# Kernel tuning notes

Hardware: AMD Instinct MI355X
Metric: run time of the kernel (lower is better)

The kernel has to match this reference:

```python
import jax, jax.numpy as jnp
import numpy as np

N = 16384        # num_nodes (64 graphs x 256 nodes, consecutive blocks)
G = 64           # num_graphs = len(nodes_per_graph)
GENES = 12132    # num_genes (hardcoded in source)
E = 262144       # edges, avg degree 16
PER = 256        # nodes per graph


def setup_inputs() -> dict:
    key = jax.random.key(0)
    ks = jax.random.split(key, 12)
    x = jax.random.normal(ks[0], (N, GENES), dtype=jnp.float32)
    edge_index = jax.random.randint(ks[1], (2, E), 0, N, dtype=jnp.int32)
    # node i belongs to graph i // PER  (consecutive-block partition as in the source loop)
    graph_ids = jnp.repeat(jnp.arange(G, dtype=jnp.int32), PER)
    node_scales = jax.random.uniform(ks[2], (GENES,), dtype=jnp.float32, minval=0.5, maxval=1.5)
    gcn_weight = jax.random.normal(ks[3], (GENES, G), dtype=jnp.float32) / np.float32(np.sqrt(GENES))
    gcn_bias = jax.random.normal(ks[4], (G,), dtype=jnp.float32) * 0.01
    w1 = jax.random.normal(ks[5], (G, N), dtype=jnp.float32) / np.float32(np.sqrt(N))   # to_graph_layer [out,in]
    b1 = jax.random.normal(ks[6], (G,), dtype=jnp.float32) * 0.01
    final_means = jax.random.normal(ks[7], (G,), dtype=jnp.float32)
    final_scales = jax.random.uniform(ks[8], (G,), dtype=jnp.float32, minval=0.5, maxval=1.5)
    w2 = jax.random.normal(ks[9], (1, G), dtype=jnp.float32) / np.float32(np.sqrt(G))   # to_final_layer
    b2 = jax.random.normal(ks[10], (1,), dtype=jnp.float32) * 0.01
    return {
        "x": x, "edge_index": edge_index, "graph_ids": graph_ids,
        "node_scales": node_scales, "gcn_weight": gcn_weight, "gcn_bias": gcn_bias,
        "w1": w1, "b1": b1, "final_means": final_means, "final_scales": final_scales,
        "w2": w2, "b2": b2,
    }


def reference(x, edge_index, graph_ids, node_scales, gcn_weight, gcn_bias,
              w1, b1, final_means, final_scales, w2, b2):
    n = x.shape[0]
    x = x / node_scales                              # [N, GENES]
    xw = x @ gcn_weight                              # [N, G]  GCNConv linear (normalize=False)
    src, dst = edge_index[0], edge_index[1]
    # message passing: sum x_j over in-edges; '+ xw' realizes the explicitly-added self loops
    agg = jax.ops.segment_sum(xw[src], dst, num_segments=n) + xw + gcn_bias  # [N, G]
    # per-graph gather: node i takes column graph_ids[i] (vectorized form of the source loop)
    selected = jnp.take_along_axis(agg, graph_ids[:, None], axis=1)[:, 0]    # [N]
    # NOTE: the (selected - graph_means)/graph_scales in the source is dead code
    # (immediately overwritten by `x = selected_outputs`), so it is omitted.
    h = w1 @ selected + b1                           # [G]
    h = (h - final_means) / final_scales
    out = w2 @ h + b2                                # [1]
    return jax.nn.sigmoid(out)
```

## Files before the change

### kernel.cpp

```cpp
#include <hip/hip_runtime.h>
#include <hip/hip_bf16.h>

typedef unsigned short u16;
typedef unsigned int   u32;
typedef __attribute__((ext_vector_type(8))) short bf16x8;
typedef __attribute__((ext_vector_type(4))) float f32x4;
typedef __attribute__((ext_vector_type(4))) u32   u32x4;

#define GENES  12132
#define KPAD   12160
#define NROW   16384
#define GCOL   64
#define BM     64
#define BK     64
#define CHUNKS 190
#define KTAIL  12096

__device__ __forceinline__ u32 pack_hi(float x, float y) {
  return __builtin_amdgcn_perm(__float_as_uint(y), __float_as_uint(x), 0x07060302u);
}
__device__ __forceinline__ u32 pack_lo(float x, float y) {
  float lx = x - __uint_as_float(__float_as_uint(x) & 0xFFFF0000u);
  float ly = y - __uint_as_float(__float_as_uint(y) & 0xFFFF0000u);
  return pack_hi(lx, ly);
}
__device__ __forceinline__ void cvt8(const float* __restrict__ p, bf16x8& h8, bf16x8& l8) {
  const f32x4 a = *(const f32x4*)p;
  const f32x4 b = *(const f32x4*)(p + 4);
  u32x4 hv = { pack_hi(a[0], a[1]), pack_hi(a[2], a[3]),
               pack_hi(b[0], b[1]), pack_hi(b[2], b[3]) };
  u32x4 lv = { pack_lo(a[0], a[1]), pack_lo(a[2], a[3]),
               pack_lo(b[0], b[1]), pack_lo(b[2], b[3]) };
  h8 = __builtin_bit_cast(bf16x8, hv);
  l8 = __builtin_bit_cast(bf16x8, lv);
}

__device__ __forceinline__ void gload16(const void* g, void* l) {
  __builtin_amdgcn_global_load_lds(
      (const __attribute__((address_space(1))) void*)g,
      (__attribute__((address_space(3))) void*)l, 16, 0, 0);
}

__global__ __launch_bounds__(256) void prep_all(
    const float* __restrict__ gw, const float* __restrict__ ns,
    const float* __restrict__ x,
    u16* __restrict__ Wth, u16* __restrict__ Wtl,
    float* __restrict__ xpad, float* __restrict__ hbuf) {
  const int bid = blockIdx.x;
  const int t   = threadIdx.x;
  if (bid < CHUNKS) {
    __shared__ u16 th[64 * 72];
    __shared__ u16 tl[64 * 72];
    const int k0 = bid * 64;
#pragma unroll
    for (int i = 0; i < 16; ++i) {
      int idx = i * 256 + t;
      int k = idx >> 6, c = idx & 63;
      int gk = k0 + k;
      float wv = 0.f;
      if (gk < GENES) wv = gw[(size_t)gk * GCOL + c] / ns[gk];
      u32 u = __float_as_uint(wv);
      float lf = wv - __uint_as_float(u & 0xFFFF0000u);
      th[c * 72 + k] = (u16)(u >> 16);
      tl[c * 72 + k] = (u16)(__float_as_uint(lf) >> 16);
    }
    __syncthreads();
    const int c  = t >> 2;
    const int kk = (t & 3) * 16;
    uint4 a0 = *(const uint4*)(th + c * 72 + kk);
    uint4 a1 = *(const uint4*)(th + c * 72 + kk + 8);
    uint4 b0 = *(const uint4*)(tl + c * 72 + kk);
    uint4 b1 = *(const uint4*)(tl + c * 72 + kk + 8);
    *(uint4*)(Wth + (size_t)c * KPAD + k0 + kk)     = a0;
    *(uint4*)(Wth + (size_t)c * KPAD + k0 + kk + 8) = a1;
    *(uint4*)(Wtl + (size_t)c * KPAD + k0 + kk)     = b0;
    *(uint4*)(Wtl + (size_t)c * KPAD + k0 + kk + 8) = b1;
  } else {
    int i = (bid - CHUNKS) * 256 + t;
    int row = i >> 6, col = i & 63;
    float v = 0.f;
    if (col < GENES - KTAIL) v = x[(size_t)row * GENES + KTAIL + col];
    xpad[i] = v;
    if (bid == CHUNKS && t < 64) hbuf[t] = 0.f;
  }
}

__global__ __launch_bounds__(512, 2) void gemm_kernel(
    const float* __restrict__ x, const float* __restrict__ xpad,
    const u16* __restrict__ Wth, const u16* __restrict__ Wtl,
    const float* __restrict__ gb,
    float* __restrict__ xw, float* __restrict__ sel) {
  __shared__ float Abuf[4][BM * BK];
  __shared__ u16   Bbuf[4][2][64 * BK];

  const int t    = threadIdx.x;
  const int W    = t >> 6;
  const int lane = t & 63;
  const int r0   = blockIdx.x * BM;

  const int arow0 = t >> 4,         acol0 = t & 15;
  const int arow1 = (512 + t) >> 4, acol1 = (512 + t) & 15;
  const int asrc0 = ((((acol0 >> 1) ^ (arow0 & 7)) << 1) | (acol0 & 1)) << 2;
  const int asrc1 = ((((acol1 >> 1) ^ (arow1 & 7)) << 1) | (acol1 & 1)) << 2;
  const int bc   = t >> 3;
  const int bsrc = ((t & 7) ^ (bc & 7)) << 3;

  const int wm = W >> 1, wn = W & 1;
  const int lr = lane & 15;
  const int kg = lane >> 4;
  const int arow = wm * 16 + lr;
  const int aridx0 = arow * 64 + (((0 * 4 + kg) ^ (arow & 7)) << 3);
  const int aridx1 = arow * 64 + (((1 * 4 + kg) ^ (arow & 7)) << 3);
  int bidx[2][2];
#pragma unroll
  for (int n2 = 0; n2 < 2; ++n2) {
    int c = (wn * 2 + n2) * 16 + lr;
#pragma unroll
    for (int s = 0; s < 2; ++s)
      bidx[n2][s] = c * 64 + (((s * 4 + kg) ^ (c & 7)) << 3);
  }

  f32x4 acc[2];
  acc[0] = (f32x4){0.f, 0.f, 0.f, 0.f};
  acc[1] = (f32x4){0.f, 0.f, 0.f, 0.f};

  auto STAGE = [&](int buf, int ch) {
    const float* Ab;
    size_t astr;
    int kof;
    if (ch < CHUNKS - 1) { Ab = x;    astr = GENES; kof = ch * BK; }
    else                 { Ab = xpad; astr = 64;    kof = 0;       }
    const int k0 = ch * BK;
    gload16(Ab + (size_t)(r0 + arow0) * astr + kof + asrc0, &Abuf[buf][(W * 64) * 4]);
    gload16(Ab + (size_t)(r0 + arow1) * astr + kof + asrc1, &Abuf[buf][(512 + W * 64) * 4]);
    gload16(Wth + (size_t)bc * KPAD + k0 + bsrc, &Bbuf[buf][0][(W * 64) * 8]);
    gload16(Wtl + (size_t)bc * KPAD + k0 + bsrc, &Bbuf[buf][1][(W * 64) * 8]);
  };

  auto COMPUTE = [&](int p) {
    bf16x8 ah0, al0, ah1, al1;
    cvt8(&Abuf[p][aridx0], ah0, al0);
    cvt8(&Abuf[p][aridx1], ah1, al1);
#pragma unroll
    for (int n2 = 0; n2 < 2; ++n2) {
      bf16x8 bh0 = *(const bf16x8*)&Bbuf[p][0][bidx[n2][0]];
      bf16x8 bl0 = *(const bf16x8*)&Bbuf[p][1][bidx[n2][0]];
      acc[n2] = __builtin_amdgcn_mfma_f32_16x16x32_bf16(ah0, bh0, acc[n2], 0, 0, 0);
      acc[n2] = __builtin_amdgcn_mfma_f32_16x16x32_bf16(al0, bh0, acc[n2], 0, 0, 0);
      acc[n2] = __builtin_amdgcn_mfma_f32_16x16x32_bf16(ah0, bl0, acc[n2], 0, 0, 0);
      bf16x8 bh1 = *(const bf16x8*)&Bbuf[p][0][bidx[n2][1]];
      bf16x8 bl1 = *(const bf16x8*)&Bbuf[p][1][bidx[n2][1]];
      acc[n2] = __builtin_amdgcn_mfma_f32_16x16x32_bf16(ah1, bh1, acc[n2], 0, 0, 0);
      acc[n2] = __builtin_amdgcn_mfma_f32_16x16x32_bf16(al1, bh1, acc[n2], 0, 0, 0);
      acc[n2] = __builtin_amdgcn_mfma_f32_16x16x32_bf16(ah1, bl1, acc[n2], 0, 0, 0);
    }
  };

  STAGE(0, 0);
  STAGE(1, 1);
  STAGE(2, 2);

  for (int ch = 0; ch < CHUNKS - 3; ++ch) {
    asm volatile("s_waitcnt vmcnt(8)" ::: "memory");
    __builtin_amdgcn_s_barrier();
    STAGE((ch + 3) & 3, ch + 3);
    COMPUTE(ch & 3);
  }
  asm volatile("s_waitcnt vmcnt(8)" ::: "memory");
  __builtin_amdgcn_s_barrier();
  COMPUTE((CHUNKS - 3) & 3);
  asm volatile("s_waitcnt vmcnt(4)" ::: "memory");
  __builtin_amdgcn_s_barrier();
  COMPUTE((CHUNKS - 2) & 3);
  asm volatile("s_waitcnt vmcnt(0)" ::: "memory");
  __builtin_amdgcn_s_barrier();
  COMPUTE((CHUNKS - 1) & 3);

  const int orow = r0 + wm * 16 + kg * 4;
#pragma unroll
  for (int n2 = 0; n2 < 2; ++n2) {
    const int col = (wn * 2 + n2) * 16 + lr;
#pragma unroll
    for (int j = 0; j < 4; ++j)
      xw[(size_t)(orow + j) * GCOL + col] = acc[n2][j];
  }
  const int g = blockIdx.x >> 2;
  if (wn == (g >> 5) && lr == (g & 15)) {
    f32x4 av = ((g >> 4) & 1) ? acc[1] : acc[0];
    float bias = gb[g];
#pragma unroll
    for (int j = 0; j < 4; ++j)
      sel[orow + j] = av[j] + bias;
  }
}

__global__ __launch_bounds__(256) void edge_kernel(
    const int* __restrict__ ei, const float* __restrict__ xw,
    float* __restrict__ sel, int E) {
  int e = blockIdx.x * 256 + threadIdx.x;
  if (e < E) {
    int s = ei[e];
    int d = ei[E + e];
    int g = d >> 8;
    atomicAdd(&sel[d], xw[(size_t)s * GCOL + g]);
  }
}

__global__ __launch_bounds__(256) void hreduce_kernel(
    const float* __restrict__ w1, const float* __restrict__ sel,
    float* __restrict__ hbuf) {
  const int k = blockIdx.x >> 2;
  const int q = blockIdx.x & 3;
  const int t = threadIdx.x;
  const float4* wr = reinterpret_cast<const float4*>(w1 + (size_t)k * NROW);
  const float4* sv = reinterpret_cast<const float4*>(sel);
  float sum = 0.f;
#pragma unroll
  for (int i = 0; i < 4; ++i) {
    int idx = q * 1024 + i * 256 + t;
    float4 a = wr[idx];
    float4 b = sv[idx];
    sum += a.x * b.x + a.y * b.y + a.z * b.z + a.w * b.w;
  }
#pragma unroll
  for (int off = 32; off > 0; off >>= 1) sum += __shfl_down(sum, off, 64);
  __shared__ float wsum[4];
  if ((t & 63) == 0) wsum[t >> 6] = sum;
  __syncthreads();
  if (t == 0) atomicAdd(&hbuf[k], wsum[0] + wsum[1] + wsum[2] + wsum[3]);
}

__global__ void finalize_kernel(
    const float* __restrict__ hbuf, const float* __restrict__ b1,
    const float* __restrict__ fm, const float* __restrict__ fs,
    const float* __restrict__ w2, const float* __restrict__ b2,
    float* __restrict__ out) {
  int t = threadIdx.x;
  float h  = hbuf[t] + b1[t];
  float hn = (h - fm[t]) / fs[t];
  float v  = w2[t] * hn;
#pragma unroll
  for (int off = 32; off > 0; off >>= 1) v += __shfl_down(v, off, 64);
  if (t == 0) {
    float z = v + b2[0];
    out[0] = 1.f / (1.f + expf(-z));
  }
}

extern "C" void kernel_launch(void* const* d_in, const int* in_sizes, int n_in,
                              void* d_out, int out_size, void* d_ws, size_t ws_size,
                              hipStream_t stream) {
  const float* x    = (const float*)d_in[0];
  const int*   ei   = (const int*)d_in[1];
  const float* ns   = (const float*)d_in[3];
  const float* gw   = (const float*)d_in[4];
  const float* gb   = (const float*)d_in[5];
  const float* w1   = (const float*)d_in[6];
  const float* b1   = (const float*)d_in[7];
  const float* fm   = (const float*)d_in[8];
  const float* fs   = (const float*)d_in[9];
  const float* w2   = (const float*)d_in[10];
  const float* b2   = (const float*)d_in[11];
  float* out = (float*)d_out;

  const int E = in_sizes[1] / 2;

  float* ws   = (float*)d_ws;
  float* xw   = ws;
  float* sel  = xw + (size_t)NROW * GCOL;
  float* hbuf = sel + NROW;
  u16*   Wth  = (u16*)(hbuf + 64);
  u16*   Wtl  = Wth + (size_t)GCOL * KPAD;
  float* xpad = (float*)(Wtl + (size_t)GCOL * KPAD);

  hipLaunchKernelGGL(prep_all, dim3(CHUNKS + NROW * 64 / 256), dim3(256), 0, stream,
                     gw, ns, x, Wth, Wtl, xpad, hbuf);
  hipLaunchKernelGGL(gemm_kernel, dim3(NROW / BM), dim3(512), 0, stream,
                     x, xpad, Wth, Wtl, gb, xw, sel);
  hipLaunchKernelGGL(edge_kernel, dim3((E + 255) / 256), dim3(256), 0, stream,
                     ei, xw, sel, E);
  hipLaunchKernelGGL(hreduce_kernel, dim3(GCOL * 4), dim3(256), 0, stream,
                     w1, sel, hbuf);
  hipLaunchKernelGGL(finalize_kernel, dim3(1), dim3(64), 0, stream,
                     hbuf, b1, fm, fs, w2, b2, out);
}
```

Baseline: 341.9 us.

## Replace LDS-pipelined GEMM with split-K single-wave direct-load kernel plus reduction

The GEMM is rewritten so each single-wave block computes a full 64x64 output tile for one fifth of the K dimension. It loads A and B straight from global memory into registers with no LDS staging or barriers. A new reduce kernel sums the five partial results, writes xw and computes the per-graph selected values with bias. The aim is more parallel blocks and no barrier overhead, at the cost of extra partial-sum traffic, one more launch, and uncoalesced per-lane global loads with no LDS reuse.

```diff
diff --git a/kernel.cpp b/kernel.cpp
--- a/kernel.cpp
+++ b/kernel.cpp
@@ -11,10 +11,10 @@
 #define KPAD   12160
 #define NROW   16384
 #define GCOL   64
-#define BM     64
-#define BK     64
-#define CHUNKS 190
 #define KTAIL  12096
+#define CHUNKS32 380
+#define KSPLIT 5
+#define CPW    76
 
 __device__ __forceinline__ u32 pack_hi(float x, float y) {
   return __builtin_amdgcn_perm(__float_as_uint(y), __float_as_uint(x), 0x07060302u);
@@ -35,12 +35,6 @@
   l8 = __builtin_bit_cast(bf16x8, lv);
 }
 
-__device__ __forceinline__ void gload16(const void* g, void* l) {
-  __builtin_amdgcn_global_load_lds(
-      (const __attribute__((address_space(1))) void*)g,
-      (__attribute__((address_space(3))) void*)l, 16, 0, 0);
-}
-
 __global__ __launch_bounds__(256) void prep_all(
     const float* __restrict__ gw, const float* __restrict__ ns,
     const float* __restrict__ x,
@@ -48,7 +42,7 @@
     float* __restrict__ xpad, float* __restrict__ hbuf) {
   const int bid = blockIdx.x;
   const int t   = threadIdx.x;
-  if (bid < CHUNKS) {
+  if (bid < KPAD / 64) {
     __shared__ u16 th[64 * 72];
     __shared__ u16 tl[64 * 72];
     const int k0 = bid * 64;
@@ -76,122 +70,96 @@
     *(uint4*)(Wtl + (size_t)c * KPAD + k0 + kk)     = b0;
     *(uint4*)(Wtl + (size_t)c * KPAD + k0 + kk + 8) = b1;
   } else {
-    int i = (bid - CHUNKS) * 256 + t;
+    int i = (bid - KPAD / 64) * 256 + t;
     int row = i >> 6, col = i & 63;
     float v = 0.f;
     if (col < GENES - KTAIL) v = x[(size_t)row * GENES + KTAIL + col];
     xpad[i] = v;
-    if (bid == CHUNKS && t < 64) hbuf[t] = 0.f;
-  }
-}
-
-__global__ __launch_bounds__(512, 2) void gemm_kernel(
+    if (bid == KPAD / 64 && t < 64) hbuf[t] = 0.f;
+  }
+}
+
+__global__ __launch_bounds__(64) void gemm_kernel(
     const float* __restrict__ x, const float* __restrict__ xpad,
     const u16* __restrict__ Wth, const u16* __restrict__ Wtl,
-    const float* __restrict__ gb,
-    float* __restrict__ xw, float* __restrict__ sel) {
-  __shared__ float Abuf[4][BM * BK];
-  __shared__ u16   Bbuf[4][2][64 * BK];
-
-  const int t    = threadIdx.x;
-  const int W    = t >> 6;
-  const int lane = t & 63;
-  const int r0   = blockIdx.x * BM;
-
-  const int arow0 = t >> 4,         acol0 = t & 15;
-  const int arow1 = (512 + t) >> 4, acol1 = (512 + t) & 15;
-  const int asrc0 = ((((acol0 >> 1) ^ (arow0 & 7)) << 1) | (acol0 & 1)) << 2;
-  const int asrc1 = ((((acol1 >> 1) ^ (arow1 & 7)) << 1) | (acol1 & 1)) << 2;
-  const int bc   = t >> 3;
-  const int bsrc = ((t & 7) ^ (bc & 7)) << 3;
-
-  const int wm = W >> 1, wn = W & 1;
-  const int lr = lane & 15;
-  const int kg = lane >> 4;
-  const int arow = wm * 16 + lr;
-  const int aridx0 = arow * 64 + (((0 * 4 + kg) ^ (arow & 7)) << 3);
-  const int aridx1 = arow * 64 + (((1 * 4 + kg) ^ (arow & 7)) << 3);
-  int bidx[2][2];
-#pragma unroll
-  for (int n2 = 0; n2 < 2; ++n2) {
-    int c = (wn * 2 + n2) * 16 + lr;
-#pragma unroll
-    for (int s = 0; s < 2; ++s)
-      bidx[n2][s] = c * 64 + (((s * 4 + kg) ^ (c & 7)) << 3);
-  }
-
-  f32x4 acc[2];
-  acc[0] = (f32x4){0.f, 0.f, 0.f, 0.f};
-  acc[1] = (f32x4){0.f, 0.f, 0.f, 0.f};
-
-  auto STAGE = [&](int buf, int ch) {
-    const float* Ab;
-    size_t astr;
-    int kof;
-    if (ch < CHUNKS - 1) { Ab = x;    astr = GENES; kof = ch * BK; }
-    else                 { Ab = xpad; astr = 64;    kof = 0;       }
-    const int k0 = ch * BK;
-    gload16(Ab + (size_t)(r0 + arow0) * astr + kof + asrc0, &Abuf[buf][(W * 64) * 4]);
-    gload16(Ab + (size_t)(r0 + arow1) * astr + kof + asrc1, &Abuf[buf][(512 + W * 64) * 4]);
-    gload16(Wth + (size_t)bc * KPAD + k0 + bsrc, &Bbuf[buf][0][(W * 64) * 8]);
-    gload16(Wtl + (size_t)bc * KPAD + k0 + bsrc, &Bbuf[buf][1][(W * 64) * 8]);
-  };
-
-  auto COMPUTE = [&](int p) {
-    bf16x8 ah0, al0, ah1, al1;
-    cvt8(&Abuf[p][aridx0], ah0, al0);
-    cvt8(&Abuf[p][aridx1], ah1, al1);
-#pragma unroll
-    for (int n2 = 0; n2 < 2; ++n2) {
-      bf16x8 bh0 = *(const bf16x8*)&Bbuf[p][0][bidx[n2][0]];
-      bf16x8 bl0 = *(const bf16x8*)&Bbuf[p][1][bidx[n2][0]];
-      acc[n2] = __builtin_amdgcn_mfma_f32_16x16x32_bf16(ah0, bh0, acc[n2], 0, 0, 0);
-      acc[n2] = __builtin_amdgcn_mfma_f32_16x16x32_bf16(al0, bh0, acc[n2], 0, 0, 0);
-      acc[n2] = __builtin_amdgcn_mfma_f32_16x16x32_bf16(ah0, bl0, acc[n2], 0, 0, 0);
-      bf16x8 bh1 = *(const bf16x8*)&Bbuf[p][0][bidx[n2][1]];
-      bf16x8 bl1 = *(const bf16x8*)&Bbuf[p][1][bidx[n2][1]];
-      acc[n2] = __builtin_amdgcn_mfma_f32_16x16x32_bf16(ah1, bh1, acc[n2], 0, 0, 0);
-      acc[n2] = __builtin_amdgcn_mfma_f32_16x16x32_bf16(al1, bh1, acc[n2], 0, 0, 0);
-      acc[n2] = __builtin_amdgcn_mfma_f32_16x16x32_bf16(ah1, bl1, acc[n2], 0, 0, 0);
-    }
-  };
-
-  STAGE(0, 0);
-  STAGE(1, 1);
-  STAGE(2, 2);
-
-  for (int ch = 0; ch < CHUNKS - 3; ++ch) {
-    asm volatile("s_waitcnt vmcnt(8)" ::: "memory");
-    __builtin_amdgcn_s_barrier();
-    STAGE((ch + 3) & 3, ch + 3);
-    COMPUTE(ch & 3);
-  }
-  asm volatile("s_waitcnt vmcnt(8)" ::: "memory");
-  __builtin_amdgcn_s_barrier();
-  COMPUTE((CHUNKS - 3) & 3);
-  asm volatile("s_waitcnt vmcnt(4)" ::: "memory");
-  __builtin_amdgcn_s_barrier();
-  COMPUTE((CHUNKS - 2) & 3);
-  asm volatile("s_waitcnt vmcnt(0)" ::: "memory");
-  __builtin_amdgcn_s_barrier();
-  COMPUTE((CHUNKS - 1) & 3);
-
-  const int orow = r0 + wm * 16 + kg * 4;
-#pragma unroll
-  for (int n2 = 0; n2 < 2; ++n2) {
-    const int col = (wn * 2 + n2) * 16 + lr;
-#pragma unroll
-    for (int j = 0; j < 4; ++j)
-      xw[(size_t)(orow + j) * GCOL + col] = acc[n2][j];
-  }
-  const int g = blockIdx.x >> 2;
-  if (wn == (g >> 5) && lr == (g & 15)) {
-    f32x4 av = ((g >> 4) & 1) ? acc[1] : acc[0];
-    float bias = gb[g];
-#pragma unroll
-    for (int j = 0; j < 4; ++j)
-      sel[orow + j] = av[j] + bias;
-  }
+    float* __restrict__ xwp) {
+  const int wid = blockIdx.x;
+  const int sp  = wid >> 8;
+  const int rg  = wid & 255;
+  const int l   = threadIdx.x;
+  const int lr  = l & 15;
+  const int kq  = l >> 4;
+
+  const int r0 = rg * 64;
+
+  f32x4 acc[4][4];
+#pragma unroll
+  for (int s = 0; s < 4; ++s)
+#pragma unroll
+    for (int c = 0; c < 4; ++c) acc[s][c] = (f32x4){0.f, 0.f, 0.f, 0.f};
+
+  const u16* bh_base = Wth + (size_t)lr * KPAD + kq * 8;
+  const u16* bl_base = Wtl + (size_t)lr * KPAD + kq * 8;
+  const int gch0 = sp * CPW;
+
+#pragma unroll 2
+  for (int ci = 0; ci < CPW; ++ci) {
+    const int gch = gch0 + ci;
+    const int k0  = gch * 32;
+    bf16x8 bh[4], bl[4];
+#pragma unroll
+    for (int cg = 0; cg < 4; ++cg) {
+      bh[cg] = *(const bf16x8*)(bh_base + (size_t)cg * (16 * KPAD) + k0);
+      bl[cg] = *(const bf16x8*)(bl_base + (size_t)cg * (16 * KPAD) + k0);
+    }
+    bf16x8 ah[4], al[4];
+    if (gch < KTAIL / 32) {
+#pragma unroll
+      for (int s = 0; s < 4; ++s)
+        cvt8(x + (size_t)(r0 + s * 16 + lr) * GENES + k0 + kq * 8, ah[s], al[s]);
+    } else {
+#pragma unroll
+      for (int s = 0; s < 4; ++s)
+        cvt8(xpad + (size_t)(r0 + s * 16 + lr) * 64 + (k0 - KTAIL) + kq * 8, ah[s], al[s]);
+    }
+#pragma unroll
+    for (int s = 0; s < 4; ++s)
+#pragma unroll
+      for (int cg = 0; cg < 4; ++cg) {
+        acc[s][cg] = __builtin_amdgcn_mfma_f32_16x16x32_bf16(ah[s], bh[cg], acc[s][cg], 0, 0, 0);
+        acc[s][cg] = __builtin_amdgcn_mfma_f32_16x16x32_bf16(al[s], bh[cg], acc[s][cg], 0, 0, 0);
+        acc[s][cg] = __builtin_amdgcn_mfma_f32_16x16x32_bf16(ah[s], bl[cg], acc[s][cg], 0, 0, 0);
+      }
+  }
+
+  float* outp = xwp + (size_t)sp * NROW * GCOL;
+#pragma unroll
+  for (int s = 0; s < 4; ++s) {
+    const int rbase = r0 + s * 16 + kq * 4;
+#pragma unroll
+    for (int cg = 0; cg < 4; ++cg) {
+      const int col = cg * 16 + lr;
+#pragma unroll
+      for (int j = 0; j < 4; ++j)
+        outp[(size_t)(rbase + j) * GCOL + col] = acc[s][cg][j];
+    }
+  }
+}
+
+__global__ __launch_bounds__(256) void reduce_sel(
+    const f32x4* __restrict__ xwp, f32x4* __restrict__ xw4,
+    const float* __restrict__ gb, float* __restrict__ sel) {
+  int i = blockIdx.x * 256 + threadIdx.x;
+  f32x4 v = xwp[i];
+#pragma unroll
+  for (int p = 1; p < KSPLIT; ++p) {
+    f32x4 u = xwp[(size_t)p * (NROW * GCOL / 4) + i];
+    v[0] += u[0]; v[1] += u[1]; v[2] += u[2]; v[3] += u[3];
+  }
+  xw4[i] = v;
+  int row = i >> 4;
+  int g = row >> 8;
+  if ((i & 15) == (g >> 2)) sel[row] = v[g & 3] + gb[g];
 }
 
 __global__ __launch_bounds__(256) void edge_kernel(
@@ -272,11 +240,14 @@
   u16*   Wth  = (u16*)(hbuf + 64);
   u16*   Wtl  = Wth + (size_t)GCOL * KPAD;
   float* xpad = (float*)(Wtl + (size_t)GCOL * KPAD);
-
-  hipLaunchKernelGGL(prep_all, dim3(CHUNKS + NROW * 64 / 256), dim3(256), 0, stream,
+  float* xwp  = xpad + (size_t)NROW * 64;
+
+  hipLaunchKernelGGL(prep_all, dim3(KPAD / 64 + NROW * 64 / 256), dim3(256), 0, stream,
                      gw, ns, x, Wth, Wtl, xpad, hbuf);
-  hipLaunchKernelGGL(gemm_kernel, dim3(NROW / BM), dim3(512), 0, stream,
-                     x, xpad, Wth, Wtl, gb, xw, sel);
+  hipLaunchKernelGGL(gemm_kernel, dim3(256 * KSPLIT), dim3(64), 0, stream,
+                     x, xpad, Wth, Wtl, xwp);
+  hipLaunchKernelGGL(reduce_sel, dim3(NROW * GCOL / 4 / 256), dim3(256), 0, stream,
+                     (const f32x4*)xwp, (f32x4*)xw, gb, sel);
   hipLaunchKernelGGL(edge_kernel, dim3((E + 255) / 256), dim3(256), 0, stream,
                      ei, xw, sel, E);
   hipLaunchKernelGGL(hreduce_kernel, dim3(GCOL * 4), dim3(256), 0, stream,
```

Result: no change. 345.7 us (+1.1%).

## Halve GEMM row tile to 32 with 256-thread blocks and triple buffering

Applied to the files above, without the earlier changes.

The GEMM block now covers 32 rows with 256 threads (4 waves) instead of 64 rows with 512 threads, so twice as many blocks are launched over the 256 CUs. The pipeline depth drops from four LDS stages to three, with a rolled loop and per-chunk waitcnt. The intent is better CU coverage and lower LDS use per block. The cost is that the W hi/lo tiles are reloaded by twice as many blocks, which doubles the B-operand traffic.

```diff
diff --git a/kernel.cpp b/kernel.cpp
--- a/kernel.cpp
+++ b/kernel.cpp
@@ -11,7 +11,7 @@
 #define KPAD   12160
 #define NROW   16384
 #define GCOL   64
-#define BM     64
+#define BM     32
 #define BK     64
 #define CHUNKS 190
 #define KTAIL  12096
@@ -48,7 +48,7 @@
     float* __restrict__ xpad, float* __restrict__ hbuf) {
   const int bid = blockIdx.x;
   const int t   = threadIdx.x;
-  if (bid < CHUNKS) {
+  if (bid < KPAD / 64) {
     __shared__ u16 th[64 * 72];
     __shared__ u16 tl[64 * 72];
     const int k0 = bid * 64;
@@ -76,34 +76,36 @@
     *(uint4*)(Wtl + (size_t)c * KPAD + k0 + kk)     = b0;
     *(uint4*)(Wtl + (size_t)c * KPAD + k0 + kk + 8) = b1;
   } else {
-    int i = (bid - CHUNKS) * 256 + t;
+    int i = (bid - KPAD / 64) * 256 + t;
     int row = i >> 6, col = i & 63;
     float v = 0.f;
     if (col < GENES - KTAIL) v = x[(size_t)row * GENES + KTAIL + col];
     xpad[i] = v;
-    if (bid == CHUNKS && t < 64) hbuf[t] = 0.f;
-  }
-}
-
-__global__ __launch_bounds__(512, 2) void gemm_kernel(
+    if (bid == KPAD / 64 && t < 64) hbuf[t] = 0.f;
+  }
+}
+
+__global__ __launch_bounds__(256, 2) void gemm_kernel(
     const float* __restrict__ x, const float* __restrict__ xpad,
     const u16* __restrict__ Wth, const u16* __restrict__ Wtl,
     const float* __restrict__ gb,
     float* __restrict__ xw, float* __restrict__ sel) {
-  __shared__ float Abuf[4][BM * BK];
-  __shared__ u16   Bbuf[4][2][64 * BK];
+  __shared__ float Abuf[3][BM * BK];
+  __shared__ u16   Bbuf[3][2][64 * BK];
 
   const int t    = threadIdx.x;
   const int W    = t >> 6;
   const int lane = t & 63;
   const int r0   = blockIdx.x * BM;
 
-  const int arow0 = t >> 4,         acol0 = t & 15;
-  const int arow1 = (512 + t) >> 4, acol1 = (512 + t) & 15;
-  const int asrc0 = ((((acol0 >> 1) ^ (arow0 & 7)) << 1) | (acol0 & 1)) << 2;
-  const int asrc1 = ((((acol1 >> 1) ^ (arow1 & 7)) << 1) | (acol1 & 1)) << 2;
-  const int bc   = t >> 3;
-  const int bsrc = ((t & 7) ^ (bc & 7)) << 3;
+  const int arow0 = t >> 4;
+  const int arow1 = 16 + (t >> 4);
+  const int acol  = t & 15;
+  const int asrc0 = ((((acol >> 1) ^ (arow0 & 7)) << 1) | (acol & 1)) << 2;
+  const int asrc1 = ((((acol >> 1) ^ (arow1 & 7)) << 1) | (acol & 1)) << 2;
+  const int bc0  = t >> 3;
+  const int bc1  = 32 + (t >> 3);
+  const int bsrc = ((t & 7) ^ (bc0 & 7)) << 3;
 
   const int wm = W >> 1, wn = W & 1;
   const int lr = lane & 15;
@@ -114,7 +116,7 @@
   int bidx[2][2];
 #pragma unroll
   for (int n2 = 0; n2 < 2; ++n2) {
-    int c = (wn * 2 + n2) * 16 + lr;
+    int c = wn * 32 + n2 * 16 + lr;
 #pragma unroll
     for (int s = 0; s < 2; ++s)
       bidx[n2][s] = c * 64 + (((s * 4 + kg) ^ (c & 7)) << 3);
@@ -131,66 +133,65 @@
     if (ch < CHUNKS - 1) { Ab = x;    astr = GENES; kof = ch * BK; }
     else                 { Ab = xpad; astr = 64;    kof = 0;       }
     const int k0 = ch * BK;
-    gload16(Ab + (size_t)(r0 + arow0) * astr + kof + asrc0, &Abuf[buf][(W * 64) * 4]);
-    gload16(Ab + (size_t)(r0 + arow1) * astr + kof + asrc1, &Abuf[buf][(512 + W * 64) * 4]);
-    gload16(Wth + (size_t)bc * KPAD + k0 + bsrc, &Bbuf[buf][0][(W * 64) * 8]);
-    gload16(Wtl + (size_t)bc * KPAD + k0 + bsrc, &Bbuf[buf][1][(W * 64) * 8]);
+    gload16(Ab + (size_t)(r0 + arow0) * astr + kof + asrc0, &Abuf[buf][t * 4]);
+    gload16(Ab + (size_t)(r0 + arow1) * astr + kof + asrc1, &Abuf[buf][(256 + t) * 4]);
+    gload16(Wth + (size_t)bc0 * KPAD + k0 + bsrc, &Bbuf[buf][0][t * 8]);
+    gload16(Wth + (size_t)bc1 * KPAD + k0 + bsrc, &Bbuf[buf][0][(256 + t) * 8]);
+    gload16(Wtl + (size_t)bc0 * KPAD + k0 + bsrc, &Bbuf[buf][1][t * 8]);
+    gload16(Wtl + (size_t)bc1 * KPAD + k0 + bsrc, &Bbuf[buf][1][(256 + t) * 8]);
   };
 
   auto COMPUTE = [&](int p) {
-    bf16x8 ah0, al0, ah1, al1;
-    cvt8(&Abuf[p][aridx0], ah0, al0);
-    cvt8(&Abuf[p][aridx1], ah1, al1);
-#pragma unroll
-    for (int n2 = 0; n2 < 2; ++n2) {
-      bf16x8 bh0 = *(const bf16x8*)&Bbuf[p][0][bidx[n2][0]];
-      bf16x8 bl0 = *(const bf16x8*)&Bbuf[p][1][bidx[n2][0]];
-      acc[n2] = __builtin_amdgcn_mfma_f32_16x16x32_bf16(ah0, bh0, acc[n2], 0, 0, 0);
-      acc[n2] = __builtin_amdgcn_mfma_f32_16x16x32_bf16(al0, bh0, acc[n2], 0, 0, 0);
-      acc[n2] = __builtin_amdgcn_mfma_f32_16x16x32_bf16(ah0, bl0, acc[n2], 0, 0, 0);
-      bf16x8 bh1 = *(const bf16x8*)&Bbuf[p][0][bidx[n2][1]];
-      bf16x8 bl1 = *(const bf16x8*)&Bbuf[p][1][bidx[n2][1]];
-      acc[n2] = __builtin_amdgcn_mfma_f32_16x16x32_bf16(ah1, bh1, acc[n2], 0, 0, 0);
-      acc[n2] = __builtin_amdgcn_mfma_f32_16x16x32_bf16(al1, bh1, acc[n2], 0, 0, 0);
-      acc[n2] = __builtin_amdgcn_mfma_f32_16x16x32_bf16(ah1, bl1, acc[n2], 0, 0, 0);
+#pragma unroll
+    for (int s = 0; s < 2; ++s) {
+      bf16x8 ah, al;
+      cvt8(&Abuf[p][s ? aridx1 : aridx0], ah, al);
+#pragma unroll
+      for (int n2 = 0; n2 < 2; ++n2) {
+        bf16x8 bh = *(const bf16x8*)&Bbuf[p][0][bidx[n2][s]];
+        bf16x8 bl = *(const bf16x8*)&Bbuf[p][1][bidx[n2][s]];
+        acc[n2] = __builtin_amdgcn_mfma_f32_16x16x32_bf16(ah, bh, acc[n2], 0, 0, 0);
+        acc[n2] = __builtin_amdgcn_mfma_f32_16x16x32_bf16(al, bh, acc[n2], 0, 0, 0);
+        acc[n2] = __builtin_amdgcn_mfma_f32_16x16x32_bf16(ah, bl, acc[n2], 0, 0, 0);
+      }
     }
   };
 
   STAGE(0, 0);
   STAGE(1, 1);
-  STAGE(2, 2);
-
-  for (int ch = 0; ch < CHUNKS - 3; ++ch) {
-    asm volatile("s_waitcnt vmcnt(8)" ::: "memory");
+
+  int p = 0;
+  for (int ch = 0; ch < CHUNKS; ++ch) {
+    if (ch == CHUNKS - 1)
+      asm volatile("s_waitcnt vmcnt(0)" ::: "memory");
+    else
+      asm volatile("s_waitcnt vmcnt(6)" ::: "memory");
     __builtin_amdgcn_s_barrier();
-    STAGE((ch + 3) & 3, ch + 3);
-    COMPUTE(ch & 3);
-  }
-  asm volatile("s_waitcnt vmcnt(8)" ::: "memory");
-  __builtin_amdgcn_s_barrier();
-  COMPUTE((CHUNKS - 3) & 3);
-  asm volatile("s_waitcnt vmcnt(4)" ::: "memory");
-  __builtin_amdgcn_s_barrier();
-  COMPUTE((CHUNKS - 2) & 3);
-  asm volatile("s_waitcnt vmcnt(0)" ::: "memory");
-  __builtin_amdgcn_s_barrier();
-  COMPUTE((CHUNKS - 1) & 3);
+    if (ch + 2 < CHUNKS) {
+      int b2 = p + 2; if (b2 >= 3) b2 -= 3;
+      STAGE(b2, ch + 2);
+    }
+    COMPUTE(p);
+    ++p; if (p == 3) p = 0;
+  }
 
   const int orow = r0 + wm * 16 + kg * 4;
 #pragma unroll
   for (int n2 = 0; n2 < 2; ++n2) {
-    const int col = (wn * 2 + n2) * 16 + lr;
+    const int col = wn * 32 + n2 * 16 + lr;
 #pragma unroll
     for (int j = 0; j < 4; ++j)
       xw[(size_t)(orow + j) * GCOL + col] = acc[n2][j];
   }
-  const int g = blockIdx.x >> 2;
-  if (wn == (g >> 5) && lr == (g & 15)) {
-    f32x4 av = ((g >> 4) & 1) ? acc[1] : acc[0];
-    float bias = gb[g];
-#pragma unroll
-    for (int j = 0; j < 4; ++j)
-      sel[orow + j] = av[j] + bias;
+  const int g = blockIdx.x >> 3;
+  const float bias = gb[g];
+#pragma unroll
+  for (int n2 = 0; n2 < 2; ++n2) {
+    if (wn * 32 + n2 * 16 + lr == g) {
+#pragma unroll
+      for (int j = 0; j < 4; ++j)
+        sel[orow + j] = acc[n2][j] + bias;
+    }
   }
 }
 
@@ -273,9 +274,9 @@
   u16*   Wtl  = Wth + (size_t)GCOL * KPAD;
   float* xpad = (float*)(Wtl + (size_t)GCOL * KPAD);
 
-  hipLaunchKernelGGL(prep_all, dim3(CHUNKS + NROW * 64 / 256), dim3(256), 0, stream,
+  hipLaunchKernelGGL(prep_all, dim3(KPAD / 64 + NROW * 64 / 256), dim3(256), 0, stream,
                      gw, ns, x, Wth, Wtl, xpad, hbuf);
-  hipLaunchKernelGGL(gemm_kernel, dim3(NROW / BM), dim3(512), 0, stream,
+  hipLaunchKernelGGL(gemm_kernel, dim3(NROW / BM), dim3(256), 0, stream,
                      x, xpad, Wth, Wtl, gb, xw, sel);
   hipLaunchKernelGGL(edge_kernel, dim3((E + 255) / 256), dim3(256), 0, stream,
                      ei, xw, sel, E);
```

Result: no change. 337.0 us (-1.4%).
